# Optimization experiments

Measured on AMD Instinct MI355X. Metric: run time of the kernel, lower is better.

Reference implementation:

```python
import jax, jax.numpy as jnp
import numpy as np

V, D, H, C = 100000, 300, 16, 5
B, T = 256, 128


def setup_inputs() -> dict:
    key = jax.random.key(0)
    ks = jax.random.split(key, 8)
    s = 1.0 / np.sqrt(H).astype(np.float32)  # PyTorch LSTM/Linear init range
    x = jax.random.randint(ks[0], (B, T), 0, V)
    emb = jax.random.normal(ks[1], (V, D), jnp.float32) * 0.02
    W_ih = jax.random.uniform(ks[2], (4 * H, D), jnp.float32, -s, s)
    W_hh = jax.random.uniform(ks[3], (4 * H, H), jnp.float32, -s, s)
    b_ih = jax.random.uniform(ks[4], (4 * H,), jnp.float32, -s, s)
    b_hh = jax.random.uniform(ks[5], (4 * H,), jnp.float32, -s, s)
    W_out = jax.random.uniform(ks[6], (C, H), jnp.float32, -s, s)
    b_out = jax.random.uniform(ks[7], (C,), jnp.float32, -s, s)
    return dict(x=x, emb=emb, W_ih=W_ih, W_hh=W_hh, b_ih=b_ih, b_hh=b_hh,
                W_out=W_out, b_out=b_out)


def reference(x, emb, W_ih, W_hh, b_ih, b_hh, W_out, b_out):
    h_dim = W_hh.shape[1]
    xe = emb[x]  # [B,T,D] embedding lookup
    # Precompute input contribution to all 4 gates for all timesteps (one big GEMM).
    xg = jnp.einsum('btd,gd->btg', xe, W_ih) + b_ih + b_hh  # [B,T,4H]
    xg = jnp.transpose(xg, (1, 0, 2))  # [T,B,4H] time-major for scan
    b = x.shape[0]
    h0 = jnp.zeros((b, h_dim), xg.dtype)
    c0 = jnp.zeros((b, h_dim), xg.dtype)

    def step(carry, g_t):
        h, c = carry
        g = g_t + h @ W_hh.T  # [B,4H]
        i, f, gg, o = jnp.split(g, 4, axis=-1)  # PyTorch gate order: i,f,g,o
        i = jax.nn.sigmoid(i)
        f = jax.nn.sigmoid(f)
        gg = jnp.tanh(gg)
        o = jax.nn.sigmoid(o)
        c = f * c + i * gg
        h = o * jnp.tanh(c)
        return (h, c), h

    _, hs = jax.lax.scan(step, (h0, c0), xg)  # hs: [T,B,H]
    hs = jnp.transpose(hs, (1, 0, 2))  # [B,T,H]
    return hs @ W_out.T + b_out  # [B,T,C]
```

## Files before the change

kernel.cpp:

```cpp
#include <hip/hip_runtime.h>
#include <cstdint>

#define BB 256
#define TT 128
#define DD 300
#define HH 16
#define GG 64
#define CC 5
#define KC 60

__global__ __launch_bounds__(256) void xg_gemm_kernel(
    const int* __restrict__ x, const float* __restrict__ emb,
    const float* __restrict__ W_ih, const float* __restrict__ b_ih,
    const float* __restrict__ b_hh, float* __restrict__ xg) {

  __shared__ float As[64 * KC];
  __shared__ float Ws[KC * 64];
  __shared__ int   xid[64];

  const int t  = threadIdx.x;
  const int tx = t & 15;
  const int ty = t >> 4;
  const int row0 = blockIdx.x * 64;

  if (t < 64) xid[t] = x[row0 + t];
  __syncthreads();

  const int na = (t < 192) ? 4 : 3;

  float4 apf[4], wpf[4];

  auto load_chunk = [&](int dbase) {
#pragma unroll
    for (int i = 0; i < 4; i++) {
      if (i < na) {
        int u = t + 256 * i;
        int r = u / 15, f = u - r * 15;
        apf[i] = *(const float4*)(emb + (size_t)xid[r] * DD + dbase + 4 * f);
      }
    }
#pragma unroll
    for (int i = 0; i < 4; i++) {
      if (i < na) {
        int u = t + 256 * i;
        int c = u / 15, f = u - c * 15;
        wpf[i] = *(const float4*)(W_ih + c * DD + dbase + 4 * f);
      }
    }
  };

  auto store_chunk = [&]() {
#pragma unroll
    for (int i = 0; i < 4; i++) {
      if (i < na) {
        int u = t + 256 * i;
        int r = u / 15, f = u - r * 15;
        *(float4*)&As[r * KC + 4 * f] = apf[i];
      }
    }
#pragma unroll
    for (int i = 0; i < 4; i++) {
      if (i < na) {
        int u = t + 256 * i;
        int c = u / 15, f = u - c * 15;
        int cp = (((c >> 2) ^ f) << 2) | (c & 3);
        const float* w = (const float*)&wpf[i];
        Ws[(4 * f + 0) * 64 + cp] = w[0];
        Ws[(4 * f + 1) * 64 + cp] = w[1];
        Ws[(4 * f + 2) * 64 + cp] = w[2];
        Ws[(4 * f + 3) * 64 + cp] = w[3];
      }
    }
  };

  float acc[4][4] = {};

  load_chunk(0);
  for (int ch = 0; ch < 5; ch++) {
    if (ch > 0) __syncthreads();
    store_chunk();
    __syncthreads();
    if (ch + 1 < 5) load_chunk((ch + 1) * KC);

#pragma unroll
    for (int q = 0; q < 15; q++) {
      float4 wc[4];
#pragma unroll
      for (int j = 0; j < 4; j++)
        wc[j] = *(const float4*)&Ws[(4 * q + j) * 64 + ((tx ^ q) << 2)];
#pragma unroll
      for (int r = 0; r < 4; r++) {
        float4 a = *(const float4*)&As[(4 * ty + r) * KC + 4 * q];
#pragma unroll
        for (int m = 0; m < 4; m++) {
          acc[r][m] = fmaf(a.x, ((const float*)&wc[0])[m], acc[r][m]);
          acc[r][m] = fmaf(a.y, ((const float*)&wc[1])[m], acc[r][m]);
          acc[r][m] = fmaf(a.z, ((const float*)&wc[2])[m], acc[r][m]);
          acc[r][m] = fmaf(a.w, ((const float*)&wc[3])[m], acc[r][m]);
        }
      }
    }
  }

  float bias[4];
#pragma unroll
  for (int m = 0; m < 4; m++)
    bias[m] = b_ih[4 * tx + m] + b_hh[4 * tx + m];

#pragma unroll
  for (int r = 0; r < 4; r++) {
    float4 o;
    o.x = acc[r][0] + bias[0];
    o.y = acc[r][1] + bias[1];
    o.z = acc[r][2] + bias[2];
    o.w = acc[r][3] + bias[3];
    *(float4*)&xg[(size_t)(row0 + 4 * ty + r) * GG + 4 * tx] = o;
  }
}

__global__ __launch_bounds__(64) void lstm_seq_kernel(
    const float* __restrict__ xg, const float* __restrict__ W_hh,
    const float* __restrict__ W_out, const float* __restrict__ b_out,
    float* __restrict__ out) {

  __shared__ float xgs[TT * GG];
  __shared__ float hsm[TT * HH];

  const int lane = threadIdx.x;
  const int b = blockIdx.x;
  const float4* __restrict__ src4 = (const float4*)(xg + (size_t)b * TT * GG);
  float4* dst4 = (float4*)xgs;

  const int k = lane >> 2;
  const int g = lane & 3;
  const int j = g * 16 + k;

  float wh[16];
  {
    const float* wr = W_hh + j * HH;
#pragma unroll
    for (int kk = 0; kk < 16; kk++) wh[kk] = wr[kk];
  }

  float4 buf[8];
#pragma unroll
  for (int i = 0; i < 8; i++) buf[i] = src4[i * 64 + lane];
#pragma unroll
  for (int i = 0; i < 8; i++) dst4[i * 64 + lane] = buf[i];

  const float L2E = 1.4426950408889634f;
  const bool is_tanh = (g == 2);
  const float gscale = is_tanh ? (-2.0f * L2E) : (-L2E);

  float c = 0.0f;
  float hu[16];
#pragma unroll
  for (int kk = 0; kk < 16; kk++) hu[kk] = 0.0f;

  for (int ch = 0; ch < 4; ch++) {
    if (ch < 3) {
#pragma unroll
      for (int i = 0; i < 8; i++)
        buf[i] = src4[(ch + 1) * 512 + i * 64 + lane];
    }

    float gp = xgs[(ch * 32) * GG + j];
#pragma unroll 4
    for (int s = 0; s < 32; s++) {
      const int ts = ch * 32 + s;
      float gn = (s < 31) ? xgs[(ts + 1) * GG + j] : 0.0f;

      float a0 = fmaf(hu[0], wh[0], gp);
      a0 = fmaf(hu[1], wh[1], a0);
      a0 = fmaf(hu[2], wh[2], a0);
      a0 = fmaf(hu[3], wh[3], a0);
      float a1 = hu[4] * wh[4];
      a1 = fmaf(hu[5], wh[5], a1);
      a1 = fmaf(hu[6], wh[6], a1);
      a1 = fmaf(hu[7], wh[7], a1);
      float a2 = hu[8] * wh[8];
      a2 = fmaf(hu[9], wh[9], a2);
      a2 = fmaf(hu[10], wh[10], a2);
      a2 = fmaf(hu[11], wh[11], a2);
      float a3 = hu[12] * wh[12];
      a3 = fmaf(hu[13], wh[13], a3);
      a3 = fmaf(hu[14], wh[14], a3);
      a3 = fmaf(hu[15], wh[15], a3);
      float gv = (a0 + a1) + (a2 + a3);

      float e = exp2f(gv * gscale);
      float sg = __builtin_amdgcn_rcpf(1.0f + e);
      float act = is_tanh ? fmaf(2.0f, sg, -1.0f) : sg;

      int ai = __float_as_int(act);
      float iv = __int_as_float(__builtin_amdgcn_update_dpp(ai, ai, 0x00, 0xF, 0xF, true));
      float fv = __int_as_float(__builtin_amdgcn_update_dpp(ai, ai, 0x55, 0xF, 0xF, true));
      float gg = __int_as_float(__builtin_amdgcn_update_dpp(ai, ai, 0xAA, 0xF, 0xF, true));
      float ov = __int_as_float(__builtin_amdgcn_update_dpp(ai, ai, 0xFF, 0xF, 0xF, true));

      c = fmaf(fv, c, iv * gg);
      float e2 = exp2f(-2.0f * L2E * c);
      float tc = fmaf(2.0f, __builtin_amdgcn_rcpf(1.0f + e2), -1.0f);
      float hnew = ov * tc;

      if (g == 0) hsm[ts * HH + k] = hnew;

#pragma unroll
      for (int kk = 0; kk < 16; kk++)
        hu[kk] = __uint_as_float(
            __builtin_amdgcn_readlane(__float_as_uint(hnew), 4 * kk));

      gp = gn;
    }

    if (ch < 3) {
#pragma unroll
      for (int i = 0; i < 8; i++)
        dst4[(ch + 1) * 512 + i * 64 + lane] = buf[i];
    }
  }

  float* outb = out + (size_t)b * TT * CC;
#pragma unroll
  for (int ii = 0; ii < 10; ii++) {
    int idx = ii * 64 + lane;
    int tt = idx / CC;
    int cc = idx - tt * CC;
    const float* wr = W_out + cc * HH;
    float accv = b_out[cc];
#pragma unroll
    for (int kk = 0; kk < 16; kk++)
      accv = fmaf(hsm[tt * HH + kk], wr[kk], accv);
    outb[idx] = accv;
  }
}

extern "C" void kernel_launch(void* const* d_in, const int* in_sizes, int n_in,
                              void* d_out, int out_size, void* d_ws, size_t ws_size,
                              hipStream_t stream) {
  const int*   x     = (const int*)d_in[0];
  const float* emb   = (const float*)d_in[1];
  const float* W_ih  = (const float*)d_in[2];
  const float* W_hh  = (const float*)d_in[3];
  const float* b_ih  = (const float*)d_in[4];
  const float* b_hh  = (const float*)d_in[5];
  const float* W_out = (const float*)d_in[6];
  const float* b_out = (const float*)d_in[7];
  float* out = (float*)d_out;
  float* xg  = (float*)d_ws;

  xg_gemm_kernel<<<BB * TT / 64, 256, 0, stream>>>(x, emb, W_ih, b_ih, b_hh, xg);
  lstm_seq_kernel<<<BB, 64, 0, stream>>>(xg, W_hh, W_out, b_out, out);
}
```

Before: 217.3 us.

## Compute input-gate GEMM with bf16x3 split MFMA instead of FP32 FMAs

Replaces the shared-memory tiled FP32 GEMM that produces the input-gate preactivations with a matrix-core version. Each FP32 operand is split into a high and a low bf16 part, and three 16x16x32 bf16 MFMAs are accumulated to approximate FP32 accuracy. A small prep kernel pre-splits W_ih into a fragment layout that lanes load directly, and embedding rows are read straight from global memory with no LDS staging. This adds an extra kernel launch and drops the lo*lo term, which slightly reduces accuracy.

```diff
diff --git a/kernel.cpp b/kernel.cpp
--- a/kernel.cpp
+++ b/kernel.cpp
@@ -7,114 +7,110 @@
 #define HH 16
 #define GG 64
 #define CC 5
-#define KC 60
-
-__global__ __launch_bounds__(256) void xg_gemm_kernel(
+#define NKS 10
+
+typedef __attribute__((ext_vector_type(8))) short short8;
+typedef __attribute__((ext_vector_type(4))) float float4v;
+
+static __device__ inline unsigned short f2bf(float f) {
+  unsigned u = __float_as_uint(f);
+  unsigned r = (u + 0x7FFFu + ((u >> 16) & 1u)) >> 16;
+  return (unsigned short)r;
+}
+static __device__ inline float bf2f(unsigned short h) {
+  return __uint_as_float(((unsigned)h) << 16);
+}
+
+__global__ __launch_bounds__(64) void w_prep_kernel(
+    const float* __restrict__ W_ih, unsigned short* __restrict__ Bh,
+    unsigned short* __restrict__ Bl) {
+  const int blk = blockIdx.x;
+  const int ks = blk >> 2, nt = blk & 3;
+  const int lane = threadIdx.x;
+  const int n = lane & 15, quad = lane >> 4;
+  const int c = nt * 16 + n;
+
+  unsigned short h8[8], l8[8];
+#pragma unroll
+  for (int j = 0; j < 8; j++) {
+    int k = ks * 32 + quad * 8 + j;
+    float v = (k < DD) ? W_ih[c * DD + k] : 0.0f;
+    unsigned short hb = f2bf(v);
+    float rem = v - bf2f(hb);
+    h8[j] = hb;
+    l8[j] = f2bf(rem);
+  }
+  size_t base = ((size_t)blk * 64 + lane) * 8;
+#pragma unroll
+  for (int j = 0; j < 8; j++) { Bh[base + j] = h8[j]; Bl[base + j] = l8[j]; }
+}
+
+__global__ __launch_bounds__(256) void xg_mfma_kernel(
     const int* __restrict__ x, const float* __restrict__ emb,
-    const float* __restrict__ W_ih, const float* __restrict__ b_ih,
-    const float* __restrict__ b_hh, float* __restrict__ xg) {
-
-  __shared__ float As[64 * KC];
-  __shared__ float Ws[KC * 64];
-  __shared__ int   xid[64];
-
-  const int t  = threadIdx.x;
-  const int tx = t & 15;
-  const int ty = t >> 4;
+    const unsigned short* __restrict__ Bh, const unsigned short* __restrict__ Bl,
+    const float* __restrict__ b_ih, const float* __restrict__ b_hh,
+    float* __restrict__ xg) {
+
+  const int t = threadIdx.x;
+  const int w = t >> 6;
+  const int lane = t & 63;
+  const int m = lane & 15, quad = lane >> 4;
   const int row0 = blockIdx.x * 64;
-
-  if (t < 64) xid[t] = x[row0 + t];
-  __syncthreads();
-
-  const int na = (t < 192) ? 4 : 3;
-
-  float4 apf[4], wpf[4];
-
-  auto load_chunk = [&](int dbase) {
-#pragma unroll
-    for (int i = 0; i < 4; i++) {
-      if (i < na) {
-        int u = t + 256 * i;
-        int r = u / 15, f = u - r * 15;
-        apf[i] = *(const float4*)(emb + (size_t)xid[r] * DD + dbase + 4 * f);
-      }
-    }
-#pragma unroll
-    for (int i = 0; i < 4; i++) {
-      if (i < na) {
-        int u = t + 256 * i;
-        int c = u / 15, f = u - c * 15;
-        wpf[i] = *(const float4*)(W_ih + c * DD + dbase + 4 * f);
-      }
-    }
-  };
-
-  auto store_chunk = [&]() {
-#pragma unroll
-    for (int i = 0; i < 4; i++) {
-      if (i < na) {
-        int u = t + 256 * i;
-        int r = u / 15, f = u - r * 15;
-        *(float4*)&As[r * KC + 4 * f] = apf[i];
-      }
-    }
-#pragma unroll
-    for (int i = 0; i < 4; i++) {
-      if (i < na) {
-        int u = t + 256 * i;
-        int c = u / 15, f = u - c * 15;
-        int cp = (((c >> 2) ^ f) << 2) | (c & 3);
-        const float* w = (const float*)&wpf[i];
-        Ws[(4 * f + 0) * 64 + cp] = w[0];
-        Ws[(4 * f + 1) * 64 + cp] = w[1];
-        Ws[(4 * f + 2) * 64 + cp] = w[2];
-        Ws[(4 * f + 3) * 64 + cp] = w[3];
-      }
-    }
-  };
-
-  float acc[4][4] = {};
-
-  load_chunk(0);
-  for (int ch = 0; ch < 5; ch++) {
-    if (ch > 0) __syncthreads();
-    store_chunk();
-    __syncthreads();
-    if (ch + 1 < 5) load_chunk((ch + 1) * KC);
-
-#pragma unroll
-    for (int q = 0; q < 15; q++) {
-      float4 wc[4];
-#pragma unroll
-      for (int j = 0; j < 4; j++)
-        wc[j] = *(const float4*)&Ws[(4 * q + j) * 64 + ((tx ^ q) << 2)];
-#pragma unroll
-      for (int r = 0; r < 4; r++) {
-        float4 a = *(const float4*)&As[(4 * ty + r) * KC + 4 * q];
-#pragma unroll
-        for (int m = 0; m < 4; m++) {
-          acc[r][m] = fmaf(a.x, ((const float*)&wc[0])[m], acc[r][m]);
-          acc[r][m] = fmaf(a.y, ((const float*)&wc[1])[m], acc[r][m]);
-          acc[r][m] = fmaf(a.z, ((const float*)&wc[2])[m], acc[r][m]);
-          acc[r][m] = fmaf(a.w, ((const float*)&wc[3])[m], acc[r][m]);
-        }
-      }
-    }
-  }
-
-  float bias[4];
-#pragma unroll
-  for (int m = 0; m < 4; m++)
-    bias[m] = b_ih[4 * tx + m] + b_hh[4 * tx + m];
-
-#pragma unroll
-  for (int r = 0; r < 4; r++) {
-    float4 o;
-    o.x = acc[r][0] + bias[0];
-    o.y = acc[r][1] + bias[1];
-    o.z = acc[r][2] + bias[2];
-    o.w = acc[r][3] + bias[3];
-    *(float4*)&xg[(size_t)(row0 + 4 * ty + r) * GG + 4 * tx] = o;
+  const int r = row0 + w * 16 + m;
+
+  const int xr = x[r];
+  const float* __restrict__ arow = emb + (size_t)xr * DD + quad * 8;
+
+  float4v acc[4];
+#pragma unroll
+  for (int nt = 0; nt < 4; nt++) acc[nt] = (float4v){0.f, 0.f, 0.f, 0.f};
+
+#pragma unroll
+  for (int ks = 0; ks < NKS; ks++) {
+    float af[8];
+    if (ks < 9) {
+      float4 a0 = *(const float4*)(arow + ks * 32);
+      float4 a1 = *(const float4*)(arow + ks * 32 + 4);
+      af[0] = a0.x; af[1] = a0.y; af[2] = a0.z; af[3] = a0.w;
+      af[4] = a1.x; af[5] = a1.y; af[6] = a1.z; af[7] = a1.w;
+    } else {
+      int k0 = 288 + quad * 8;
+      float4 a0 = (k0 + 4 <= DD) ? *(const float4*)(arow + ks * 32)
+                                 : (float4){0.f, 0.f, 0.f, 0.f};
+      float4 a1 = (k0 + 8 <= DD) ? *(const float4*)(arow + ks * 32 + 4)
+                                 : (float4){0.f, 0.f, 0.f, 0.f};
+      af[0] = a0.x; af[1] = a0.y; af[2] = a0.z; af[3] = a0.w;
+      af[4] = a1.x; af[5] = a1.y; af[6] = a1.z; af[7] = a1.w;
+    }
+
+    short8 ah, al;
+#pragma unroll
+    for (int j = 0; j < 8; j++) {
+      unsigned short hb = f2bf(af[j]);
+      ah[j] = (short)hb;
+      al[j] = (short)f2bf(af[j] - bf2f(hb));
+    }
+
+#pragma unroll
+    for (int nt = 0; nt < 4; nt++) {
+      size_t fo = ((size_t)(ks * 4 + nt) * 64 + lane) * 8;
+      short8 bh = *(const short8*)(Bh + fo);
+      short8 bl = *(const short8*)(Bl + fo);
+      acc[nt] = __builtin_amdgcn_mfma_f32_16x16x32_bf16(ah, bh, acc[nt], 0, 0, 0);
+      acc[nt] = __builtin_amdgcn_mfma_f32_16x16x32_bf16(al, bh, acc[nt], 0, 0, 0);
+      acc[nt] = __builtin_amdgcn_mfma_f32_16x16x32_bf16(ah, bl, acc[nt], 0, 0, 0);
+    }
+  }
+
+#pragma unroll
+  for (int nt = 0; nt < 4; nt++) {
+    int col = nt * 16 + m;
+    float bias = b_ih[col] + b_hh[col];
+#pragma unroll
+    for (int reg = 0; reg < 4; reg++) {
+      int rs = row0 + w * 16 + quad * 4 + reg;
+      xg[(size_t)rs * GG + col] = acc[nt][reg] + bias;
+    }
   }
 }
 
@@ -247,8 +243,12 @@
   const float* W_out = (const float*)d_in[6];
   const float* b_out = (const float*)d_in[7];
   float* out = (float*)d_out;
-  float* xg  = (float*)d_ws;
-
-  xg_gemm_kernel<<<BB * TT / 64, 256, 0, stream>>>(x, emb, W_ih, b_ih, b_hh, xg);
+
+  float* xg = (float*)d_ws;
+  unsigned short* Bh = (unsigned short*)((char*)d_ws + (size_t)BB * TT * GG * 4);
+  unsigned short* Bl = Bh + NKS * 4 * 64 * 8;
+
+  w_prep_kernel<<<NKS * 4, 64, 0, stream>>>(W_ih, Bh, Bl);
+  xg_mfma_kernel<<<BB * TT / 64, 256, 0, stream>>>(x, emb, Bh, Bl, b_ih, b_hh, xg);
   lstm_seq_kernel<<<BB, 64, 0, stream>>>(xg, W_hh, W_out, b_out, out);
 }
```

Result: faster. 211.4 us (-2.7%).
